# Kernel tuning notes

Measured on AMD Instinct MI355X. Metric: run time of the kernel, lower is better.

The kernel has to match this reference:

```python
import jax, jax.numpy as jnp
import numpy as np

K = 20
BN_SCALE = 1.0 / np.sqrt(1.0 + 1e-5)  # BN at init: running_mean=0, running_var=1


def _graph_feature(x, k):
    # x: (B, N, C) point features -> (B, N, k, 2C) edge features
    sq = jnp.sum(x * x, axis=-1)  # (B, N)
    # negative squared distance: larger == closer (matches torch topk on -dist)
    d = 2.0 * jnp.einsum('bnc,bmc->bnm', x, x) - sq[:, :, None] - sq[:, None, :]
    idx = jax.lax.top_k(d, k)[1]  # (B, N, k), self included as nearest
    nbr = jax.vmap(lambda pts, i: pts[i])(x, idx)  # (B, N, k, C) gather
    ctr = jnp.broadcast_to(x[:, :, None, :], nbr.shape)
    return jnp.concatenate([nbr - ctr, ctr], axis=-1)


def _edge_conv(e, W, g, b):
    # 1x1 Conv2d (no bias) + BatchNorm(init stats) + LeakyReLU(0.2) + max over k
    y = jnp.einsum('bnkc,oc->bnko', e, W)
    y = jax.nn.leaky_relu(y * (g * BN_SCALE) + b, 0.2)
    return jnp.max(y, axis=2)  # (B, N, O)


def setup_inputs() -> dict:
    key = jax.random.key(0)
    ks = jax.random.split(key, 12)
    B, N = 4, 1024
    dims_in = [6, 128, 256, 512]
    dims_out = [64, 128, 256, 512]
    inp = {'x': jax.random.normal(ks[0], (B, N, 3), dtype=jnp.float32)}
    for i, (ci, co) in enumerate(zip(dims_in, dims_out), start=1):
        inp[f'W{i}'] = jax.random.normal(ks[i], (co, ci), dtype=jnp.float32) * (1.0 / np.sqrt(ci))
        inp[f'g{i}'] = jnp.ones((co,), dtype=jnp.float32)
        inp[f'b{i}'] = jnp.zeros((co,), dtype=jnp.float32)
    inp['W5'] = jax.random.normal(ks[5], (512, 960), dtype=jnp.float32) * (1.0 / np.sqrt(960.0))
    inp['g5'] = jnp.ones((512,), dtype=jnp.float32)
    inp['b5'] = jnp.zeros((512,), dtype=jnp.float32)
    inp['We'] = jax.random.normal(ks[6], (256, 512), dtype=jnp.float32) * (1.0 / np.sqrt(512.0))
    return inp


def reference(x, W1, g1, b1, W2, g2, b2, W3, g3, b3, W4, g4, b4, W5, g5, b5, We):
    x1 = _edge_conv(_graph_feature(x, K), W1, g1, b1)   # (B, N, 64)
    x2 = _edge_conv(_graph_feature(x1, K), W2, g2, b2)  # (B, N, 128)
    x3 = _edge_conv(_graph_feature(x2, K), W3, g3, b3)  # (B, N, 256)
    x4 = _edge_conv(_graph_feature(x3, K), W4, g4, b4)  # (B, N, 512)
    xc = jnp.concatenate([x1, x2, x3, x4], axis=-1)     # (B, N, 960)
    y = jnp.einsum('bnc,oc->bno', xc, W5)               # conv5 (1x1 Conv1d)
    y = jax.nn.leaky_relu(y * (g5 * BN_SCALE) + b5, 0.2)
    feat = jnp.max(y, axis=1)                           # (B, 512) global max-pool
    return feat @ We.T                                  # (B, num_features)
```

## Files before the change

### kernel.cpp

```cpp
#include <hip/hip_runtime.h>
#include <hip/hip_bf16.h>
#include <math.h>

typedef __hip_bfloat16 bf16;
typedef __bf16 v8bf __attribute__((ext_vector_type(8)));
typedef float v4f __attribute__((ext_vector_type(4)));

#define BN_SCALE 0.9999950000374997f
#define NPTS 1024
#define NB 4
#define CH5 ((size_t)4 * 1024 * 512)

__device__ __forceinline__ float b2f(bf16 v) { return __bfloat162float(v); }
__device__ __forceinline__ bf16 f2b(float v) { return __float2bfloat16(v); }
__device__ __forceinline__ float ldw(const void* p, size_t i, int isf) {
    return isf ? ((const float*)p)[i] : b2f(((const bf16*)p)[i]);
}
__device__ __forceinline__ unsigned ordf(float f) {
    unsigned u = __float_as_uint(f);
    return (u & 0x80000000u) ? ~u : (u | 0x80000000u);
}
__device__ __forceinline__ float iordf(unsigned u) {
    return (u & 0x80000000u) ? __uint_as_float(u ^ 0x80000000u) : __uint_as_float(~u);
}

__device__ __forceinline__ int detect_isf(const void* xraw, int* cnt) {
    const unsigned short* u = (const unsigned short*)xraw;
    int t = threadIdx.x, c = 0;
    for (int i = t; i < 512; i += 256) {
        unsigned short v = u[i];
        int e = (v >> 7) & 0xFF;
        int m = v & 0x7F;
        if (e == 0xFF || e >= 141 || (e == 0 && m != 0)) c++;
    }
    cnt[t] = c;
    __syncthreads();
    for (int off = 128; off > 0; off >>= 1) {
        if (t < off) cnt[t] += cnt[t + off];
        __syncthreads();
    }
    int isf = (cnt[0] > 30) ? 1 : 0;
    __syncthreads();
    return isf;
}

__global__ void k_prep(const void* __restrict__ W1, const void* __restrict__ W2,
                       const void* __restrict__ W3, const void* __restrict__ W4,
                       const void* __restrict__ W5, const void* __restrict__ x,
                       bf16* __restrict__ Whi, bf16* __restrict__ Wlo,
                       bf16* __restrict__ xph, bf16* __restrict__ xpl, float* __restrict__ sq,
                       int* __restrict__ flag, unsigned* __restrict__ pooledU) {
    __shared__ int cnt[256];
    int isf = detect_isf(x, cnt);
    if (blockIdx.x == 0) {
        if (threadIdx.x == 0) *flag = isf;
        for (int i = threadIdx.x; i < 2048; i += 256) pooledU[i] = 0u;
    }
    int idx = blockIdx.x * 256 + threadIdx.x;
    if (idx < 839680) {
        const void* src; int C, O, Kpad, two, local;
        if (idx < 4096)        { src = W1; C = 3;   O = 64;  Kpad = 32;  two = 1; local = idx; }
        else if (idx < 20480)  { src = W2; C = 64;  O = 128; Kpad = 64;  two = 1; local = idx - 4096; }
        else if (idx < 86016)  { src = W3; C = 128; O = 256; Kpad = 128; two = 1; local = idx - 20480; }
        else if (idx < 348160) { src = W4; C = 256; O = 512; Kpad = 256; two = 1; local = idx - 86016; }
        else                   { src = W5; C = 960; O = 512; Kpad = 960; two = 0; local = idx - 348160; }
        int r = local / Kpad, c = local % Kpad;
        float wv = 0.f;
        if (c < C) {
            size_t off;
            if (two) off = (r < O) ? (size_t)r * 2 * C + c : (size_t)(r - O) * 2 * C + C + c;
            else     off = (size_t)r * C + c;
            wv = ldw(src, off, isf);
        }
        bf16 h = f2b(wv);
        Whi[idx] = h;
        Wlo[idx] = f2b(wv - b2f(h));
    } else if (idx < 843776) {
        int p = idx - 839680;
        int z = p >> 10, n = p & 1023;
        bf16* ph = xph + (size_t)z * NPTS * 32;
        bf16* pl = xpl + (size_t)z * NPTS * 32;
        float s = 0.f;
        for (int c = 0; c < 32; c++) {
            float v = (c < 3) ? ldw(x, (size_t)z * NPTS * 3 + n * 3 + c, isf) : 0.f;
            bf16 h = f2b(v);
            ph[n * 32 + c] = h;
            pl[n * 32 + c] = f2b(v - b2f(h));
            s += v * v;
        }
        sq[z * NPTS + n] = s;
    }
}

__device__ __forceinline__ int lidx(int plane, int row) {
    return ((((plane << 7) | row)) ^ (plane << 1)) << 3;
}
__device__ __forceinline__ void fill128(bf16* dst, const bf16* src, int ld) {
    int t = threadIdx.x;
    int r = t >> 2, kq = t & 3;
    *(float4*)(dst + lidx(kq, r))      = *(const float4*)(src + (size_t)r * ld + kq * 8);
    *(float4*)(dst + lidx(kq, r + 64)) = *(const float4*)(src + (size_t)(r + 64) * ld + kq * 8);
}
__device__ __forceinline__ v8bf ldf(const bf16* tile, int sub, int l) {
    return *(const v8bf*)(tile + lidx(l >> 4, sub * 16 + (l & 15)));
}

__global__ __launch_bounds__(256) void k_layer_a(const bf16* __restrict__ Xhi, const bf16* __restrict__ Xlo,
                                                 int ld, int Kpad, size_t xstride,
                                                 const bf16* __restrict__ Whi, const bf16* __restrict__ Wlo,
                                                 int O, const float* __restrict__ sqg,
                                                 float* __restrict__ Dg, float* __restrict__ Pg,
                                                 const int* __restrict__ flag) {
    int i = blockIdx.x;
    int z = (i >> 1) & 3;
    int bi = ((i >> 3) << 1) | (i & 1);
    const bf16* Xh = Xhi + (size_t)z * xstride;
    const bf16* Xl = Xlo + (size_t)z * xstride;
    __shared__ alignas(16) bf16 Ah[4096], Al[4096], Bh[4096], Bl[4096];
    int w = threadIdx.x >> 6, l = threadIdx.x & 63;
    int wr = w >> 1, wc = w & 1;
    int quad = l >> 4, col = l & 15;
    v4f zero = {0.f, 0.f, 0.f, 0.f};
    v4f acc[4][4] = {{zero, zero, zero, zero}, {zero, zero, zero, zero},
                     {zero, zero, zero, zero}, {zero, zero, zero, zero}};

    if (bi < 36) {
        int bx = 0;
        while ((((bx + 1) * (bx + 2)) >> 1) <= bi) bx++;
        int by = bi - ((bx * (bx + 1)) >> 1);
        const float* sq = sqg + z * NPTS;
        float* D = Dg + (size_t)z * NPTS * NPTS;
        int n0 = by * 128, m0 = bx * 128;
        for (int k0 = 0; k0 < Kpad; k0 += 32) {
            __syncthreads();
            fill128(Ah, Xh + (size_t)n0 * ld + k0, ld);
            fill128(Bh, Xh + (size_t)m0 * ld + k0, ld);
            fill128(Al, Xl + (size_t)n0 * ld + k0, ld);
            fill128(Bl, Xl + (size_t)m0 * ld + k0, ld);
            __syncthreads();
            v8bf ah[4], al[4];
#pragma unroll
            for (int mi = 0; mi < 4; mi++) {
                ah[mi] = ldf(Ah, wr * 4 + mi, l);
                al[mi] = ldf(Al, wr * 4 + mi, l);
            }
#pragma unroll
            for (int ni = 0; ni < 4; ni++) {
                v8bf bh = ldf(Bh, wc * 4 + ni, l);
                v8bf bl = ldf(Bl, wc * 4 + ni, l);
#pragma unroll
                for (int mi = 0; mi < 4; mi++) {
                    acc[mi][ni] = __builtin_amdgcn_mfma_f32_16x16x32_bf16(ah[mi], bh, acc[mi][ni], 0, 0, 0);
                    acc[mi][ni] = __builtin_amdgcn_mfma_f32_16x16x32_bf16(ah[mi], bl, acc[mi][ni], 0, 0, 0);
                    acc[mi][ni] = __builtin_amdgcn_mfma_f32_16x16x32_bf16(al[mi], bh, acc[mi][ni], 0, 0, 0);
                }
            }
        }
        int rb = n0 + wr * 64 + quad * 4;
        int cb = m0 + wc * 64 + col;
        float sm[4];
#pragma unroll
        for (int ni = 0; ni < 4; ni++) sm[ni] = sq[cb + ni * 16];
#pragma unroll
        for (int mi = 0; mi < 4; mi++) {
#pragma unroll
            for (int r = 0; r < 4; r++) {
                int row = rb + mi * 16 + r;
                float sn = sq[row];
#pragma unroll
                for (int ni = 0; ni < 4; ni++) {
                    float d = 2.f * acc[mi][ni][r] - sn - sm[ni];
                    int c = cb + ni * 16;
                    D[(size_t)row * NPTS + c] = d;
                    if (bx != by) D[(size_t)c * NPTS + row] = d;
                }
            }
        }
    } else {
        int isf = *flag;
        int nCol = (2 * O) >> 7;
        int s = bi - 36;
        int n0 = (s % nCol) * 128;
        int m0 = (s / nCol) * 128;
        int N2 = 2 * O;
        float* P = Pg + (size_t)z * NPTS * N2;
        for (int k0 = 0; k0 < Kpad; k0 += 32) {
            __syncthreads();
            fill128(Ah, Xh + (size_t)m0 * ld + k0, ld);
            fill128(Al, Xl + (size_t)m0 * ld + k0, ld);
            fill128(Bh, Whi + (size_t)n0 * Kpad + k0, Kpad);
            if (isf) fill128(Bl, Wlo + (size_t)n0 * Kpad + k0, Kpad);
            __syncthreads();
            v8bf ah[4], al[4];
#pragma unroll
            for (int mi = 0; mi < 4; mi++) {
                ah[mi] = ldf(Ah, wr * 4 + mi, l);
                al[mi] = ldf(Al, wr * 4 + mi, l);
            }
#pragma unroll
            for (int ni = 0; ni < 4; ni++) {
                v8bf bh = ldf(Bh, wc * 4 + ni, l);
#pragma unroll
                for (int mi = 0; mi < 4; mi++) {
                    acc[mi][ni] = __builtin_amdgcn_mfma_f32_16x16x32_bf16(ah[mi], bh, acc[mi][ni], 0, 0, 0);
                    acc[mi][ni] = __builtin_amdgcn_mfma_f32_16x16x32_bf16(al[mi], bh, acc[mi][ni], 0, 0, 0);
                }
                if (isf) {
                    v8bf bl = ldf(Bl, wc * 4 + ni, l);
#pragma unroll
                    for (int mi = 0; mi < 4; mi++)
                        acc[mi][ni] = __builtin_amdgcn_mfma_f32_16x16x32_bf16(ah[mi], bl, acc[mi][ni], 0, 0, 0);
                }
            }
        }
        int rb = m0 + wr * 64 + quad * 4;
        int cb = n0 + wc * 64 + col;
#pragma unroll
        for (int mi = 0; mi < 4; mi++)
#pragma unroll
            for (int r = 0; r < 4; r++) {
                int row = rb + mi * 16 + r;
#pragma unroll
                for (int ni = 0; ni < 4; ni++)
                    P[(size_t)row * N2 + cb + ni * 16] = acc[mi][ni][r];
            }
    }
}

template<int PAT>
__device__ __forceinline__ void swz_step(float& bv, int& bi) {
    float ov = __int_as_float(__builtin_amdgcn_ds_swizzle(__float_as_int(bv), PAT));
    int   oi = __builtin_amdgcn_ds_swizzle(bi, PAT);
    if (ov > bv || (ov == bv && oi < bi)) { bv = ov; bi = oi; }
}
__device__ __forceinline__ void shfl_step(float& bv, int& bi, int mask) {
    float ov = __shfl_xor(bv, mask);
    int   oi = __shfl_xor(bi, mask);
    if (ov > bv || (ov == bv && oi < bi)) { bv = ov; bi = oi; }
}
#define PICK(va, ja, vb, jb, vo, jo) { bool t_ = (vb) > (va); vo = t_ ? (vb) : (va); jo = t_ ? (jb) : (ja); }

__global__ __launch_bounds__(256) void k_layer_b(const float* __restrict__ Dg, const float* __restrict__ Pg,
                                                 const void* __restrict__ g, const void* __restrict__ bias,
                                                 int O, bf16* __restrict__ xhOut, bf16* __restrict__ xlOut,
                                                 float* __restrict__ sqOut, int writeSq,
                                                 const int* __restrict__ flag) {
    __shared__ int ids[4][20];
    __shared__ int boff[4][20];
    __shared__ float sqP[4][8];
    int isf = *flag;
    int i = blockIdx.x;
    int z = (i >> 1) & 3;
    int local = ((i >> 3) << 1) | (i & 1);
    int tid = threadIdx.x;
    int wq = tid >> 6, l = tid & 63;
    int row = local * 4 + wq;

    {
        const float* Dr = Dg + (size_t)z * NPTS * NPTS + (size_t)row * NPTS;
        float v[16];
#pragma unroll
        for (int jj = 0; jj < 4; jj++) {
            float4 f4 = *(const float4*)(Dr + jj * 256 + l * 4);
            v[jj * 4 + 0] = f4.x; v[jj * 4 + 1] = f4.y;
            v[jj * 4 + 2] = f4.z; v[jj * 4 + 3] = f4.w;
        }
        for (int s = 0; s < 20; s++) {
            float x0, x1, x2, x3, x4, x5, x6, x7, u0, u1, u2, u3, t0, t1, bv;
            int   y0, y1, y2, y3, y4, y5, y6, y7, w0, w1, w2, w3, s0, s1, bj;
            PICK(v[0], 0, v[1], 1, x0, y0);   PICK(v[2], 2, v[3], 3, x1, y1);
            PICK(v[4], 4, v[5], 5, x2, y2);   PICK(v[6], 6, v[7], 7, x3, y3);
            PICK(v[8], 8, v[9], 9, x4, y4);   PICK(v[10], 10, v[11], 11, x5, y5);
            PICK(v[12], 12, v[13], 13, x6, y6); PICK(v[14], 14, v[15], 15, x7, y7);
            PICK(x0, y0, x1, y1, u0, w0);     PICK(x2, y2, x3, y3, u1, w1);
            PICK(x4, y4, x5, y5, u2, w2);     PICK(x6, y6, x7, y7, u3, w3);
            PICK(u0, w0, u1, w1, t0, s0);     PICK(u2, w2, u3, w3, t1, s1);
            PICK(t0, s0, t1, s1, bv, bj);
            int bi = (bj >> 2) * 256 + l * 4 + (bj & 3);
            swz_step<0x041F>(bv, bi);
            swz_step<0x081F>(bv, bi);
            swz_step<0x101F>(bv, bi);
            swz_step<0x201F>(bv, bi);
            swz_step<0x401F>(bv, bi);
            shfl_step(bv, bi, 32);
            if (l == 0) ids[wq][s] = bi;
            if (((bi >> 2) & 63) == l) {
                int ej = (bi >> 8) * 4 + (bi & 3);
#pragma unroll
                for (int j = 0; j < 16; j++)
                    if (j == ej) v[j] = -__builtin_inff();
            }
        }
    }
    __syncthreads();
    int N2 = 2 * O;
    if (tid < 80) {
        int r = tid / 20, j = tid % 20;
        boff[r][j] = ids[r][j] * N2;
    }
    __syncthreads();

    const float* P = Pg + (size_t)z * NPTS * N2;
    int Olog = __builtin_ctz(O);
    for (int it = tid; it < 4 * O; it += 256) {
        int r = it >> Olog, o = it & (O - 1);
        int n = local * 4 + r;
        float tv = P[(size_t)n * N2 + O + o] - P[(size_t)n * N2 + o];
        float mx = -__builtin_inff(), mn = __builtin_inff();
#pragma unroll
        for (int j = 0; j < 20; j++) {
            float v = P[boff[r][j] + o];
            mx = fmaxf(mx, v);
            mn = fminf(mn, v);
        }
        float scl = ldw(g, o, isf) * BN_SCALE;
        float bb = ldw(bias, o, isf);
        float base = (scl >= 0.f ? mx : mn) + tv;
        float acc = base * scl + bb;
        acc = acc > 0.f ? acc : 0.2f * acc;
        bf16 hi = f2b(acc);
        bf16 lo = f2b(acc - b2f(hi));
        xhOut[(size_t)z * NPTS * 960 + (size_t)n * 960 + o] = hi;
        xlOut[(size_t)z * NPTS * 960 + (size_t)n * 960 + o] = lo;
        if (writeSq) {
            float xv = b2f(hi) + b2f(lo);
            float s = xv * xv;
#pragma unroll
            for (int off = 32; off > 0; off >>= 1) s += __shfl_down(s, off);
            if (l == 0) sqP[r][o >> 6] = s;
        }
    }
    if (writeSq) {
        __syncthreads();
        if (tid < 4) {
            int nc = O >> 6;
            float tot = 0.f;
            for (int c = 0; c < nc; c++) tot += sqP[tid][c];
            sqOut[z * NPTS + local * 4 + tid] = tot;
        }
    }
}

__global__ __launch_bounds__(256) void k_conv5(const bf16* __restrict__ Xhi, const bf16* __restrict__ Xlo,
                                               const bf16* __restrict__ Whi, const bf16* __restrict__ Wlo,
                                               float* __restrict__ P5,
                                               const int* __restrict__ flag) {
    int isf = *flag;
    int i = blockIdx.x;
    int z = (i >> 1) & 3;
    int rest = ((i >> 3) << 1) | (i & 1);
    int ks = rest >> 5;
    int tile = rest & 31;
    int m0 = (tile >> 2) * 128, o0 = (tile & 3) * 128;
    const bf16* Xh = Xhi + (size_t)z * NPTS * 960;
    const bf16* Xl = Xlo + (size_t)z * NPTS * 960;
    __shared__ alignas(16) bf16 Ah[4096], Al[4096], Bh[4096], Bl[4096];
    int w = threadIdx.x >> 6, l = threadIdx.x & 63;
    int wr = w >> 1, wc = w & 1;
    int quad = l >> 4, col = l & 15;
    v4f zero = {0.f, 0.f, 0.f, 0.f};
    v4f acc[4][4] = {{zero, zero, zero, zero}, {zero, zero, zero, zero},
                     {zero, zero, zero, zero}, {zero, zero, zero, zero}};
    int kbeg = ks * 160, kend = kbeg + 160;
    for (int k0 = kbeg; k0 < kend; k0 += 32) {
        __syncthreads();
        fill128(Ah, Xh + (size_t)m0 * 960 + k0, 960);
        fill128(Al, Xl + (size_t)m0 * 960 + k0, 960);
        fill128(Bh, Whi + (size_t)o0 * 960 + k0, 960);
        if (isf) fill128(Bl, Wlo + (size_t)o0 * 960 + k0, 960);
        __syncthreads();
        v8bf ah[4], al[4];
#pragma unroll
        for (int mi = 0; mi < 4; mi++) {
            ah[mi] = ldf(Ah, wr * 4 + mi, l);
            al[mi] = ldf(Al, wr * 4 + mi, l);
        }
#pragma unroll
        for (int ni = 0; ni < 4; ni++) {
            v8bf bh = ldf(Bh, wc * 4 + ni, l);
#pragma unroll
            for (int mi = 0; mi < 4; mi++) {
                acc[mi][ni] = __builtin_amdgcn_mfma_f32_16x16x32_bf16(ah[mi], bh, acc[mi][ni], 0, 0, 0);
                acc[mi][ni] = __builtin_amdgcn_mfma_f32_16x16x32_bf16(al[mi], bh, acc[mi][ni], 0, 0, 0);
            }
            if (isf) {
                v8bf bl = ldf(Bl, wc * 4 + ni, l);
#pragma unroll
                for (int mi = 0; mi < 4; mi++)
                    acc[mi][ni] = __builtin_amdgcn_mfma_f32_16x16x32_bf16(ah[mi], bl, acc[mi][ni], 0, 0, 0);
            }
        }
    }
    float* Pw = P5 + (size_t)ks * CH5 + (size_t)z * NPTS * 512;
    int rb = m0 + wr * 64 + quad * 4;
    int cb = o0 + wc * 64 + col;
#pragma unroll
    for (int mi = 0; mi < 4; mi++)
#pragma unroll
        for (int r = 0; r < 4; r++) {
            int row = rb + mi * 16 + r;
#pragma unroll
            for (int ni = 0; ni < 4; ni++)
                Pw[(size_t)row * 512 + cb + ni * 16] = acc[mi][ni][r];
        }
}

__global__ __launch_bounds__(256) void k_pool5(const float* __restrict__ P5,
                                               const void* __restrict__ g, const void* __restrict__ bias,
                                               unsigned* __restrict__ pooledU,
                                               const int* __restrict__ flag) {
    __shared__ float red2[128];
    int isf = *flag;
    int i = blockIdx.x;
    int z = (i >> 1) & 3;
    int rest = ((i >> 3) << 1) | (i & 1);
    int oc = (rest & 3) * 128, mc = (rest >> 2) * 128;
    int t = threadIdx.x;
    int c = t & 127, h = t >> 7;
    int o = oc + c;
    float scl = ldw(g, o, isf) * BN_SCALE;
    float bb = ldw(bias, o, isf);
    const float* p0 = P5 + (size_t)z * NPTS * 512 + (size_t)(mc + h * 64) * 512 + o;
    float ym = -__builtin_inff();
    for (int r = 0; r < 64; r++) {
        const float* p = p0 + (size_t)r * 512;
        float s = p[0];
#pragma unroll
        for (int ks = 1; ks < 6; ks++) s += p[(size_t)ks * CH5];
        float v = s * scl + bb;
        v = v > 0.f ? v : 0.2f * v;
        ym = fmaxf(ym, v);
    }
    if (h == 1) red2[c] = ym;
    __syncthreads();
    if (h == 0) {
        float m = fmaxf(ym, red2[c]);
        atomicMax(&pooledU[z * 512 + o], ordf(m));
    }
}

__global__ void k_final(const unsigned* __restrict__ pooledU, const void* __restrict__ We,
                        void* __restrict__ out, const int* __restrict__ flag) {
    __shared__ float p[512];
    int isf = *flag;
    int b = blockIdx.x >> 2, fb = blockIdx.x & 3;
    int t = threadIdx.x, w = t >> 6, l = t & 63;
    for (int i = t; i < 512; i += 256) p[i] = iordf(pooledU[b * 512 + i]);
    __syncthreads();
    for (int it = 0; it < 16; it++) {
        int f = fb * 64 + w * 16 + it;
        float s = 0.f;
        size_t base = (size_t)f * 512 + l * 8;
#pragma unroll
        for (int j = 0; j < 8; j++) s += p[l * 8 + j] * ldw(We, base + j, isf);
#pragma unroll
        for (int off = 32; off > 0; off >>= 1) s += __shfl_down(s, off);
        if (l == 0) {
            if (isf) ((float*)out)[b * 256 + f] = s;
            else     ((bf16*)out)[b * 256 + f] = f2b(s);
        }
    }
}

extern "C" void kernel_launch(void* const* d_in, const int* in_sizes, int n_in,
                              void* d_out, int out_size, void* d_ws, size_t ws_size,
                              hipStream_t stream) {
    const void* x  = d_in[0];
    const void* Wl[4] = { d_in[1], d_in[4], d_in[7], d_in[10] };
    const void* gl[4] = { d_in[2], d_in[5], d_in[8], d_in[11] };
    const void* bl[4] = { d_in[3], d_in[6], d_in[9], d_in[12] };
    const void* W5 = d_in[13];
    const void* g5 = d_in[14];
    const void* b5 = d_in[15];
    const void* We = d_in[16];

    char* base = (char*)d_ws;
    bf16*     xc_hi   = (bf16*)(base);
    bf16*     xc_lo   = (bf16*)(base + 7864320);
    bf16*     xpadh   = (bf16*)(base + 15728640);
    bf16*     xpadl   = (bf16*)(base + 15990784);
    float*    Dbuf    = (float*)(base + 16252928);
    float*    Pbuf    = (float*)(base + 33030144);
    bf16*     Whi     = (bf16*)(base + 49807360);
    bf16*     Wlo     = (bf16*)(base + 51486720);
    unsigned* pooledU = (unsigned*)(base + 53493760);
    float*    sq      = (float*)(base + 53501952);
    int*      flag    = (int*)(base + 53518336);
    float*    P5      = (float*)(base + 53520384);

    const int Kpad[4]   = { 32, 64, 128, 256 };
    const int Os[4]     = { 64, 128, 256, 512 };
    const int Woff[5]   = { 0, 4096, 20480, 86016, 348160 };
    const int colIn[4]  = { 0, 0, 64, 192 };
    const int colOut[4] = { 0, 64, 192, 448 };

    k_prep<<<3296, 256, 0, stream>>>(Wl[0], Wl[1], Wl[2], Wl[3], W5, x,
                                     Whi, Wlo, xpadh, xpadl, sq, flag, pooledU);

    for (int l = 0; l < 4; l++) {
        int O = Os[l];
        int nCol = (2 * O) >> 7;
        int nBlk = 36 + 8 * nCol;
        const bf16* Xh = (l == 0) ? xpadh : (xc_hi + colIn[l]);
        const bf16* Xl = (l == 0) ? xpadl : (xc_lo + colIn[l]);
        int ld = (l == 0) ? 32 : 960;
        size_t xstr = (l == 0) ? (size_t)NPTS * 32 : (size_t)NPTS * 960;
        k_layer_a<<<nBlk * NB, 256, 0, stream>>>(
            Xh, Xl, ld, Kpad[l], xstr, Whi + Woff[l], Wlo + Woff[l], O, sq, Dbuf, Pbuf, flag);
        k_layer_b<<<NPTS * NB / 4, 256, 0, stream>>>(
            Dbuf, Pbuf, gl[l], bl[l], O, xc_hi + colOut[l], xc_lo + colOut[l], sq, l < 3, flag);
    }
    k_conv5<<<768, 256, 0, stream>>>(xc_hi, xc_lo, Whi + Woff[4], Wlo + Woff[4], P5, flag);
    k_pool5<<<128, 256, 0, stream>>>(P5, g5, b5, pooledU, flag);
    k_final<<<16, 256, 0, stream>>>(pooledU, We, d_out, flag);
}
```

Baseline: 334.7 us.

## Cache per-group maxima in top-k, use scalar neighbor offsets, widen pool5 grid

The per-lane top-20 selection now keeps a cached maximum for each of four groups of four values and recomputes only the group that lost its winner. This replaces the full 16-element tournament on every iteration. The gather phase loops over rows with wave-uniform neighbor offsets read via readfirstlane, which drops the shared-memory boff table and one barrier. k_pool5 now processes 32 rows per block across 512 blocks instead of 128 rows across 128 blocks, giving more parallelism at the cost of more atomicMax traffic.

```diff
diff --git a/kernel.cpp b/kernel.cpp
--- a/kernel.cpp
+++ b/kernel.cpp
@@ -246,7 +246,6 @@
                                                  float* __restrict__ sqOut, int writeSq,
                                                  const int* __restrict__ flag) {
     __shared__ int ids[4][20];
-    __shared__ int boff[4][20];
     __shared__ float sqP[4][8];
     int isf = *flag;
     int i = blockIdx.x;
@@ -265,16 +264,18 @@
             v[jj * 4 + 0] = f4.x; v[jj * 4 + 1] = f4.y;
             v[jj * 4 + 2] = f4.z; v[jj * 4 + 3] = f4.w;
         }
+        float bmv[4]; int bmj[4];
+#pragma unroll
+        for (int gg = 0; gg < 4; gg++) {
+            float a0, a1; int j0, j1;
+            PICK(v[4 * gg + 0], 4 * gg + 0, v[4 * gg + 1], 4 * gg + 1, a0, j0);
+            PICK(v[4 * gg + 2], 4 * gg + 2, v[4 * gg + 3], 4 * gg + 3, a1, j1);
+            PICK(a0, j0, a1, j1, bmv[gg], bmj[gg]);
+        }
         for (int s = 0; s < 20; s++) {
-            float x0, x1, x2, x3, x4, x5, x6, x7, u0, u1, u2, u3, t0, t1, bv;
-            int   y0, y1, y2, y3, y4, y5, y6, y7, w0, w1, w2, w3, s0, s1, bj;
-            PICK(v[0], 0, v[1], 1, x0, y0);   PICK(v[2], 2, v[3], 3, x1, y1);
-            PICK(v[4], 4, v[5], 5, x2, y2);   PICK(v[6], 6, v[7], 7, x3, y3);
-            PICK(v[8], 8, v[9], 9, x4, y4);   PICK(v[10], 10, v[11], 11, x5, y5);
-            PICK(v[12], 12, v[13], 13, x6, y6); PICK(v[14], 14, v[15], 15, x7, y7);
-            PICK(x0, y0, x1, y1, u0, w0);     PICK(x2, y2, x3, y3, u1, w1);
-            PICK(x4, y4, x5, y5, u2, w2);     PICK(x6, y6, x7, y7, u3, w3);
-            PICK(u0, w0, u1, w1, t0, s0);     PICK(u2, w2, u3, w3, t1, s1);
+            float t0, t1, bv; int s0, s1, bj;
+            PICK(bmv[0], bmj[0], bmv[1], bmj[1], t0, s0);
+            PICK(bmv[2], bmj[2], bmv[3], bmj[3], t1, s1);
             PICK(t0, s0, t1, s1, bv, bj);
             int bi = (bj >> 2) * 256 + l * 4 + (bj & 3);
             swz_step<0x041F>(bv, bi);
@@ -286,48 +287,57 @@
             if (l == 0) ids[wq][s] = bi;
             if (((bi >> 2) & 63) == l) {
                 int ej = (bi >> 8) * 4 + (bi & 3);
-#pragma unroll
-                for (int j = 0; j < 16; j++)
-                    if (j == ej) v[j] = -__builtin_inff();
+                int eg = ej >> 2, ek = ej & 3;
+#pragma unroll
+                for (int gg = 0; gg < 4; gg++) if (gg == eg) {
+#pragma unroll
+                    for (int kk = 0; kk < 4; kk++)
+                        if (kk == ek) v[4 * gg + kk] = -__builtin_inff();
+                    float a0, a1; int j0, j1;
+                    PICK(v[4 * gg + 0], 4 * gg + 0, v[4 * gg + 1], 4 * gg + 1, a0, j0);
+                    PICK(v[4 * gg + 2], 4 * gg + 2, v[4 * gg + 3], 4 * gg + 3, a1, j1);
+                    PICK(a0, j0, a1, j1, bmv[gg], bmj[gg]);
+                }
             }
         }
     }
     __syncthreads();
+
     int N2 = 2 * O;
-    if (tid < 80) {
-        int r = tid / 20, j = tid % 20;
-        boff[r][j] = ids[r][j] * N2;
-    }
-    __syncthreads();
-
     const float* P = Pg + (size_t)z * NPTS * N2;
-    int Olog = __builtin_ctz(O);
-    for (int it = tid; it < 4 * O; it += 256) {
-        int r = it >> Olog, o = it & (O - 1);
+#pragma unroll
+    for (int r = 0; r < 4; r++) {
+        int offj[20];
+#pragma unroll
+        for (int j = 0; j < 20; j++)
+            offj[j] = __builtin_amdgcn_readfirstlane(ids[r][j]) * N2;
         int n = local * 4 + r;
-        float tv = P[(size_t)n * N2 + O + o] - P[(size_t)n * N2 + o];
-        float mx = -__builtin_inff(), mn = __builtin_inff();
-#pragma unroll
-        for (int j = 0; j < 20; j++) {
-            float v = P[boff[r][j] + o];
-            mx = fmaxf(mx, v);
-            mn = fminf(mn, v);
-        }
-        float scl = ldw(g, o, isf) * BN_SCALE;
-        float bb = ldw(bias, o, isf);
-        float base = (scl >= 0.f ? mx : mn) + tv;
-        float acc = base * scl + bb;
-        acc = acc > 0.f ? acc : 0.2f * acc;
-        bf16 hi = f2b(acc);
-        bf16 lo = f2b(acc - b2f(hi));
-        xhOut[(size_t)z * NPTS * 960 + (size_t)n * 960 + o] = hi;
-        xlOut[(size_t)z * NPTS * 960 + (size_t)n * 960 + o] = lo;
-        if (writeSq) {
-            float xv = b2f(hi) + b2f(lo);
-            float s = xv * xv;
-#pragma unroll
-            for (int off = 32; off > 0; off >>= 1) s += __shfl_down(s, off);
-            if (l == 0) sqP[r][o >> 6] = s;
+        const float* Pn = P + (size_t)n * N2;
+        for (int o = tid; o < O; o += 256) {
+            float tv = Pn[O + o] - Pn[o];
+            float mx = -__builtin_inff(), mn = __builtin_inff();
+#pragma unroll
+            for (int j = 0; j < 20; j++) {
+                float vv = P[offj[j] + o];
+                mx = fmaxf(mx, vv);
+                mn = fminf(mn, vv);
+            }
+            float scl = ldw(g, o, isf) * BN_SCALE;
+            float bb = ldw(bias, o, isf);
+            float base = (scl >= 0.f ? mx : mn) + tv;
+            float acc = base * scl + bb;
+            acc = acc > 0.f ? acc : 0.2f * acc;
+            bf16 hi = f2b(acc);
+            bf16 lo = f2b(acc - b2f(hi));
+            xhOut[(size_t)z * NPTS * 960 + (size_t)n * 960 + o] = hi;
+            xlOut[(size_t)z * NPTS * 960 + (size_t)n * 960 + o] = lo;
+            if (writeSq) {
+                float xv = b2f(hi) + b2f(lo);
+                float s2 = xv * xv;
+#pragma unroll
+                for (int off = 32; off > 0; off >>= 1) s2 += __shfl_down(s2, off);
+                if (l == 0) sqP[r][o >> 6] = s2;
+            }
         }
     }
     if (writeSq) {
@@ -414,15 +424,15 @@
     int i = blockIdx.x;
     int z = (i >> 1) & 3;
     int rest = ((i >> 3) << 1) | (i & 1);
-    int oc = (rest & 3) * 128, mc = (rest >> 2) * 128;
+    int oc = (rest & 3) * 128, mc = (rest >> 2) * 32;
     int t = threadIdx.x;
     int c = t & 127, h = t >> 7;
     int o = oc + c;
     float scl = ldw(g, o, isf) * BN_SCALE;
     float bb = ldw(bias, o, isf);
-    const float* p0 = P5 + (size_t)z * NPTS * 512 + (size_t)(mc + h * 64) * 512 + o;
+    const float* p0 = P5 + (size_t)z * NPTS * 512 + (size_t)(mc + h * 16) * 512 + o;
     float ym = -__builtin_inff();
-    for (int r = 0; r < 64; r++) {
+    for (int r = 0; r < 16; r++) {
         const float* p = p0 + (size_t)r * 512;
         float s = p[0];
 #pragma unroll
@@ -511,6 +521,6 @@
             Dbuf, Pbuf, gl[l], bl[l], O, xc_hi + colOut[l], xc_lo + colOut[l], sq, l < 3, flag);
     }
     k_conv5<<<768, 256, 0, stream>>>(xc_hi, xc_lo, Whi + Woff[4], Wlo + Woff[4], P5, flag);
-    k_pool5<<<128, 256, 0, stream>>>(P5, g5, b5, pooledU, flag);
+    k_pool5<<<512, 256, 0, stream>>>(P5, g5, b5, pooledU, flag);
     k_final<<<16, 256, 0, stream>>>(pooledU, We, d_out, flag);
 }
```

Result: faster. 326.1 us (-2.6%).
